# Optimization experiments

Measured on AMD Instinct MI355X. Metric: run time of the kernel, lower is better.

## Reference

```python
import jax, jax.numpy as jnp
import numpy as np

IN_F = 1024
OUT_F = 4096
SEARCH_SPACE = [1, 2, 4, 8, 16]  # block sizes; powers of 2 dividing both dims, capped at 16


def circ_avg(W, bs):
    """Project W [out,in] onto block-circulant structure with block size bs.

    Equivalent to trans_to_cir_meng: within each (bs x bs) block, average each
    wrap-around diagonal and rebuild a circulant block C[k, j] = c[(k - j) % bs].
    """
    q, p = W.shape[0] // bs, W.shape[1] // bs
    t = W.reshape(q, bs, p, bs).transpose(0, 2, 1, 3)  # [q, p, bs, bs]
    i = jnp.arange(bs)
    # rot[..., i, j] = t[..., i, (i + j) % bs]  (rotate rows so diagonals align in columns)
    rot = t[:, :, i[:, None], (i[:, None] + i[None, :]) % bs]  # [q, p, bs, bs]
    c = rot.mean(axis=2)  # [q, p, bs]  mean over each diagonal
    # circulant block: w[..., k, j] = c[..., (k - j) % bs]
    w = c[:, :, (i[:, None] - i[None, :]) % bs]  # [q, p, bs, bs]
    return w.transpose(0, 2, 1, 3).reshape(W.shape)


def setup_inputs() -> dict:
    key = jax.random.key(0)
    k1, k2, k3, k4 = jax.random.split(key, 4)
    x = jax.random.normal(k1, (16, 512, IN_F), dtype=jnp.float32)
    weight = jax.random.normal(k2, (OUT_F, IN_F), dtype=jnp.float32) * 0.02
    alphas = jax.random.normal(k3, (len(SEARCH_SPACE),), dtype=jnp.float32)
    bias = jax.random.normal(k4, (OUT_F,), dtype=jnp.float32) * 0.02
    return {"x": x, "weight": weight, "alphas": alphas, "bias": bias}


def reference(x, weight, alphas, bias):
    # soft NAS mixture over block sizes (tau=1, soft mode)
    a = jax.nn.softmax(alphas)
    W = a[0] * weight  # block_size 1 == original weight
    for idx, bs in enumerate(SEARCH_SPACE[1:], start=1):
        W = W + a[idx] * circ_avg(weight, bs)
    # F.linear: y = x @ W^T + b
    return jnp.einsum("bsi,oi->bso", x, W) + bias
```

## Files before the change

kernel.cpp:

```cpp
#include <hip/hip_runtime.h>

typedef __bf16 bf16;
typedef __bf16 bf16x8 __attribute__((ext_vector_type(8)));
typedef float floatx4 __attribute__((ext_vector_type(4)));

#define IN_F  1024
#define OUT_F 4096
#define M_DIM 8192
#define K_DIM 1024
#define N_DIM 4096

__device__ __forceinline__ unsigned short f2bf(float f) {
    unsigned int u = __float_as_uint(f);
    u += 0x7FFFu + ((u >> 16) & 1u);
    return (unsigned short)(u >> 16);
}

__global__ __launch_bounds__(256) void prep_kernel(
    const float* __restrict__ W, const float* __restrict__ alphas,
    const float* __restrict__ x,
    unsigned short* __restrict__ Wb, uint4* __restrict__ xb)
{
    const int t = threadIdx.x;

    if (blockIdx.x >= 1024) {
        const int g = (blockIdx.x - 1024) * 256 + t;
        const float4* xv = (const float4*)x;
        const float4 v0 = xv[2 * g];
        const float4 v1 = xv[2 * g + 1];
        uint4 o;
        o.x = (unsigned)f2bf(v0.x) | ((unsigned)f2bf(v0.y) << 16);
        o.y = (unsigned)f2bf(v0.z) | ((unsigned)f2bf(v0.w) << 16);
        o.z = (unsigned)f2bf(v1.x) | ((unsigned)f2bf(v1.y) << 16);
        o.w = (unsigned)f2bf(v1.z) | ((unsigned)f2bf(v1.w) << 16);
        xb[g] = o;
        return;
    }

    __shared__ __align__(16) float Wl[16 * 256];
    __shared__ __align__(16) float D2[2048];
    __shared__ float D4[1024];
    __shared__ float D8[512];
    __shared__ float D16[256];

    const int rb = blockIdx.x >> 2;
    const int cb = blockIdx.x & 3;
    const int row0 = rb * 16, col0 = cb * 256;

    const float4* src = (const float4*)(W + (size_t)row0 * IN_F + col0);
    #pragma unroll
    for (int j = 0; j < 4; ++j) {
        const int idx = j * 256 + t;
        const int r = idx >> 6, c4 = idx & 63;
        ((float4*)Wl)[r * 64 + c4] = src[(size_t)r * 256 + c4];
    }

    float av[5];
    float mx = -1e30f;
    #pragma unroll
    for (int j = 0; j < 5; ++j) { av[j] = alphas[j]; mx = fmaxf(mx, av[j]); }
    float s = 0.f;
    #pragma unroll
    for (int j = 0; j < 5; ++j) { av[j] = __expf(av[j] - mx); s += av[j]; }
    const float inv = 1.f / s;
    #pragma unroll
    for (int j = 0; j < 5; ++j) av[j] *= inv;
    #pragma unroll
    for (int e = 1; e <= 4; ++e) av[e] *= 1.0f / (float)(1 << e);

    __syncthreads();

    {   const int c16 = t >> 4, d = t & 15;
        float acc = 0.f;
        #pragma unroll
        for (int r = 0; r < 16; ++r)
            acc += Wl[r * 256 + c16 * 16 + ((r + d) & 15)];
        D16[t] = acc;
    }
    #pragma unroll
    for (int it = 0; it < 2; ++it) {
        const int s8 = t + it * 256;
        const int d = s8 & 7, c8 = (s8 >> 3) & 31, r8 = s8 >> 8;
        float acc = 0.f;
        #pragma unroll
        for (int r = 0; r < 8; ++r)
            acc += Wl[(r8 * 8 + r) * 256 + c8 * 8 + ((r + d) & 7)];
        D8[s8] = acc;
    }
    #pragma unroll
    for (int it = 0; it < 4; ++it) {
        const int s4 = t + it * 256;
        const int d = s4 & 3, c4 = (s4 >> 2) & 63, r4 = s4 >> 8;
        float acc = 0.f;
        #pragma unroll
        for (int r = 0; r < 4; ++r)
            acc += Wl[(r4 * 4 + r) * 256 + c4 * 4 + ((r + d) & 3)];
        D4[s4] = acc;
    }
    #pragma unroll
    for (int it = 0; it < 8; ++it) {
        const int s2 = t + it * 256;
        const int d = s2 & 1, c2 = (s2 >> 1) & 127, r2 = s2 >> 8;
        D2[s2] = Wl[(r2 * 2) * 256 + c2 * 2 + d]
               + Wl[(r2 * 2 + 1) * 256 + c2 * 2 + ((1 + d) & 1)];
    }

    __syncthreads();

    const int k = t >> 4, jj = t & 15;
    float res[16];
    #pragma unroll
    for (int jb = 0; jb < 16; ++jb) {
        const int col = jb * 16 + jj;
        const int dd = k - col;
        res[jb] = av[0] * Wl[k * 256 + col]
                + av[1] * D2[((k >> 1) * 128 + (col >> 1)) * 2 + (dd & 1)]
                + av[2] * D4[((k >> 2) * 64  + (col >> 2)) * 4 + (dd & 3)]
                + av[3] * D8[((k >> 3) * 32  + (col >> 3)) * 8 + (dd & 7)]
                + av[4] * D16[(col >> 4) * 16 + (dd & 15)];
    }

    __syncthreads();
    unsigned short* st = (unsigned short*)D2;
    #pragma unroll
    for (int jb = 0; jb < 16; ++jb)
        st[k * 256 + jb * 16 + jj] = f2bf(res[jb]);
    __syncthreads();

    const uint4* p = (const uint4*)(st + k * 256 + jj * 16);
    uint4* dst = (uint4*)(Wb + (size_t)(row0 + k) * IN_F + col0 + jj * 16);
    dst[0] = p[0];
    dst[1] = p[1];
}

#define GTM 256
#define GTN 128
#define GTK 32
#define A_EL (GTM * GTK)
#define B_EL (GTN * GTK)
#define BUF_EL (A_EL + B_EL)

__global__ __launch_bounds__(256, 2) void gemm_bt_kernel(
    const bf16* __restrict__ A, const bf16* __restrict__ B,
    const float* __restrict__ bias, float* __restrict__ C)
{
    constexpr int N = N_DIM, K = K_DIM;
    constexpr int NT = K / GTK;

    __shared__ __align__(16) bf16 smem[2 * BUF_EL];

    const int t    = threadIdx.x;
    const int w    = t >> 6;
    const int l    = t & 63;
    const int quad = l >> 4;
    const int l16  = l & 15;

    const int wm = (w >> 1) * 128;
    const int wn = (w & 1) * 64;

    const int nb = N / GTN;
    const int bm = blockIdx.x / nb;
    const int bn = blockIdx.x % nb;

    const int fko = l16 * GTK + ((quad ^ ((l16 >> 1) & 3)) * 8);

    const bf16* Ag[4]; int la[4];
    const bf16* Bg[2]; int lb[2];
    {
        const bf16* Abase = A + (size_t)bm * GTM * K;
        const bf16* Bbase = B + (size_t)bn * GTN * K;
        #pragma unroll
        for (int q = 0; q < 4; ++q) {
            const int c = q * 256 + t;
            const int row = c >> 2;
            const int kq = (c & 3) ^ ((row >> 1) & 3);
            Ag[q] = Abase + (size_t)row * K + kq * 8;
            la[q] = (q * 256 + (t & ~63)) * 8;
        }
        #pragma unroll
        for (int q = 0; q < 2; ++q) {
            const int c = q * 256 + t;
            const int row = c >> 2;
            const int kq = (c & 3) ^ ((row >> 1) & 3);
            Bg[q] = Bbase + (size_t)row * K + kq * 8;
            lb[q] = (q * 256 + (t & ~63)) * 8;
        }
    }

    floatx4 acc[8][4] = {};

#define GLL(SRC, DST)                                                         \
    __builtin_amdgcn_global_load_lds(                                         \
        (const __attribute__((address_space(1))) void*)(SRC),                 \
        (__attribute__((address_space(3))) void*)(DST), 16, 0, 0)

#define STAGE(KOFF, BUFP) do {                                                \
        _Pragma("unroll")                                                     \
        for (int q = 0; q < 4; ++q) GLL(Ag[q] + (KOFF), (BUFP) + la[q]);      \
        _Pragma("unroll")                                                     \
        for (int q = 0; q < 2; ++q) GLL(Bg[q] + (KOFF), (BUFP) + A_EL + lb[q]); \
    } while (0)

#define MF(d, va, vb)                                                         \
    d = __builtin_amdgcn_mfma_f32_16x16x32_bf16(va, vb, d, 0, 0, 0)

    STAGE(0, smem);

    #pragma unroll 1
    for (int kt = 0; kt < NT; ++kt) {
        bf16* cur = smem + (kt & 1) * BUF_EL;
        bf16* nxt = smem + ((kt & 1) ^ 1) * BUF_EL;

        if (kt < NT - 1) {
            STAGE((kt + 1) * GTK, nxt);
            asm volatile("s_waitcnt vmcnt(6)" ::: "memory");
        } else {
            asm volatile("s_waitcnt vmcnt(0)" ::: "memory");
        }
        __builtin_amdgcn_s_barrier();

        bf16x8 af[8], bfr[4];
        const bf16* a0 = cur + wm * GTK + fko;
        const bf16* b0 = cur + A_EL + wn * GTK + fko;
        #pragma unroll
        for (int n = 0; n < 4; ++n)
            bfr[n] = *(const bf16x8*)(b0 + n * 16 * GTK);
        #pragma unroll
        for (int m = 0; m < 8; ++m)
            af[m] = *(const bf16x8*)(a0 + m * 16 * GTK);

        __builtin_amdgcn_s_setprio(1);
        #pragma unroll
        for (int m = 0; m < 8; ++m)
            #pragma unroll
            for (int n = 0; n < 4; ++n)
                MF(acc[m][n], af[m], bfr[n]);
        __builtin_amdgcn_s_setprio(0);

        __builtin_amdgcn_s_barrier();
    }
#undef STAGE
#undef GLL
#undef MF

    float bv[4];
    #pragma unroll
    for (int nt = 0; nt < 4; ++nt)
        bv[nt] = bias[bn * GTN + wn + nt * 16 + l16];

    float* Cbase = C + (size_t)(bm * GTM + wm) * N + bn * GTN + wn;
    #pragma unroll
    for (int m = 0; m < 8; ++m) {
        #pragma unroll
        for (int r = 0; r < 4; ++r) {
            float* crowp = Cbase + (size_t)(m * 16 + quad * 4 + r) * N;
            #pragma unroll
            for (int nt = 0; nt < 4; ++nt)
                crowp[nt * 16 + l16] = acc[m][nt][r] + bv[nt];
        }
    }
}

extern "C" void kernel_launch(void* const* d_in, const int* in_sizes, int n_in,
                              void* d_out, int out_size, void* d_ws, size_t ws_size,
                              hipStream_t stream) {
    const float* x      = (const float*)d_in[0];
    const float* weight = (const float*)d_in[1];
    const float* alphas = (const float*)d_in[2];
    const float* bias   = (const float*)d_in[3];
    float* out = (float*)d_out;

    unsigned short* Wb = (unsigned short*)d_ws;
    unsigned short* Xb = (unsigned short*)((char*)d_ws + (size_t)OUT_F * IN_F * 2);

    prep_kernel<<<1024 + 4096, 256, 0, stream>>>(weight, alphas, x, Wb, (uint4*)Xb);

    const int grid = (M_DIM / GTM) * (N_DIM / GTN);
    gemm_bt_kernel<<<grid, 256, 0, stream>>>((const bf16*)Xb, (const bf16*)Wb, bias, out);
}
```

Before: 226.9 us.

## Restructure GEMM into 256x256x64 tiles with 8 waves and staged interleaved prefetch

The bf16 GEMM moves from 256x128x32 tiles with 4 waves to 256x256x64 tiles with 8 waves. The K loop is unrolled into sub-phases that interleave LDS fragment reads, MFMA groups and global-to-LDS prefetch of the next A half-tiles and the B tiles two steps ahead, over a double-buffered 128KB LDS. The goal is more reuse per tile, fewer K iterations and better overlap of loads with matrix math. The cost is many more barriers per tile, and the large LDS footprint combined with launch bounds of 2 may limit occupancy.

```diff
diff --git a/kernel.cpp b/kernel.cpp
--- a/kernel.cpp
+++ b/kernel.cpp
@@ -133,21 +133,17 @@
     dst[1] = p[1];
 }
 
-#define GTM 256
-#define GTN 128
-#define GTK 32
-#define A_EL (GTM * GTK)
-#define B_EL (GTN * GTK)
-#define BUF_EL (A_EL + B_EL)
-
-__global__ __launch_bounds__(256, 2) void gemm_bt_kernel(
+#define BK2 64
+#define HEL 8192
+#define SEL (4 * HEL)
+
+__global__ __launch_bounds__(512, 2) void gemm_bt_kernel(
     const bf16* __restrict__ A, const bf16* __restrict__ B,
     const float* __restrict__ bias, float* __restrict__ C)
 {
     constexpr int N = N_DIM, K = K_DIM;
-    constexpr int NT = K / GTK;
-
-    __shared__ __align__(16) bf16 smem[2 * BUF_EL];
+
+    __shared__ __align__(16) bf16 smem[2 * SEL];
 
     const int t    = threadIdx.x;
     const int w    = t >> 6;
@@ -155,100 +151,119 @@
     const int quad = l >> 4;
     const int l16  = l & 15;
 
-    const int wm = (w >> 1) * 128;
-    const int wn = (w & 1) * 64;
-
-    const int nb = N / GTN;
-    const int bm = blockIdx.x / nb;
-    const int bn = blockIdx.x % nb;
-
-    const int fko = l16 * GTK + ((quad ^ ((l16 >> 1) & 3)) * 8);
-
-    const bf16* Ag[4]; int la[4];
-    const bf16* Bg[2]; int lb[2];
-    {
-        const bf16* Abase = A + (size_t)bm * GTM * K;
-        const bf16* Bbase = B + (size_t)bn * GTN * K;
-        #pragma unroll
-        for (int q = 0; q < 4; ++q) {
-            const int c = q * 256 + t;
-            const int row = c >> 2;
-            const int kq = (c & 3) ^ ((row >> 1) & 3);
-            Ag[q] = Abase + (size_t)row * K + kq * 8;
-            la[q] = (q * 256 + (t & ~63)) * 8;
-        }
-        #pragma unroll
-        for (int q = 0; q < 2; ++q) {
-            const int c = q * 256 + t;
-            const int row = c >> 2;
-            const int kq = (c & 3) ^ ((row >> 1) & 3);
-            Bg[q] = Bbase + (size_t)row * K + kq * 8;
-            lb[q] = (q * 256 + (t & ~63)) * 8;
-        }
-    }
+    const int wr = w >> 2;
+    const int wc = w & 3;
+    const int wm = wr * 128;
+    const int wn = wc * 64;
+
+    const int bm = blockIdx.x >> 4;
+    const int bn = blockIdx.x & 15;
+
+    const int fk0 = ((0 * 4 + quad) ^ (l16 & 7)) * 8;
+    const int fk1 = ((1 * 4 + quad) ^ (l16 & 7)) * 8;
+    const int arow = wr * HEL + l16 * 64;
+    const int brow = (2 + (wc >> 1)) * HEL + ((wc & 1) * 64 + l16) * 64;
+
+    const int r0  = t >> 3;
+    const int kc0 = ((t & 7) ^ (r0 & 7)) * 8;
+    const bf16* pA = A + (size_t)(bm * 256 + r0) * K + kc0;
+    const bf16* pB = B + (size_t)(bn * 256 + r0) * K + kc0;
+    const int t8 = t * 8;
 
     floatx4 acc[8][4] = {};
-
-#define GLL(SRC, DST)                                                         \
+    bf16x8 af[4][2], bfr[4][2];
+
+#define GLL(SRC, DSTOFF)                                                      \
     __builtin_amdgcn_global_load_lds(                                         \
         (const __attribute__((address_space(1))) void*)(SRC),                 \
-        (__attribute__((address_space(3))) void*)(DST), 16, 0, 0)
-
-#define STAGE(KOFF, BUFP) do {                                                \
+        (__attribute__((address_space(3))) void*)(smem + (DSTOFF)), 16, 0, 0)
+
+#define STAGE_A(H, TT, SL) do {                                               \
+    GLL(pA + (size_t)(H) * 128 * K + (TT) * BK2,          (SL) + (H) * HEL + t8);        \
+    GLL(pA + (size_t)(H) * 128 * K + 64 * K + (TT) * BK2, (SL) + (H) * HEL + 4096 + t8); \
+} while (0)
+#define STAGE_B(H, TT, SL) do {                                               \
+    GLL(pB + (size_t)(H) * 128 * K + (TT) * BK2,          (SL) + (2 + (H)) * HEL + t8);        \
+    GLL(pB + (size_t)(H) * 128 * K + 64 * K + (TT) * BK2, (SL) + (2 + (H)) * HEL + 4096 + t8); \
+} while (0)
+
+#define RD_A(MB, SC) do { _Pragma("unroll")                                   \
+    for (int mi = 0; mi < 4; ++mi) {                                          \
+        af[mi][0] = *(const bf16x8*)(smem + (SC) + arow + ((MB) + mi) * 1024 + fk0); \
+        af[mi][1] = *(const bf16x8*)(smem + (SC) + arow + ((MB) + mi) * 1024 + fk1); \
+    } } while (0)
+#define RD_B(NB, SC) do { _Pragma("unroll")                                   \
+    for (int ni = 0; ni < 2; ++ni) {                                          \
+        bfr[(NB) + ni][0] = *(const bf16x8*)(smem + (SC) + brow + ((NB) + ni) * 1024 + fk0); \
+        bfr[(NB) + ni][1] = *(const bf16x8*)(smem + (SC) + brow + ((NB) + ni) * 1024 + fk1); \
+    } } while (0)
+
+#define MFMA16(MB, NB) do {                                                   \
+    __builtin_amdgcn_s_setprio(1);                                            \
+    _Pragma("unroll")                                                         \
+    for (int mi = 0; mi < 4; ++mi)                                            \
         _Pragma("unroll")                                                     \
-        for (int q = 0; q < 4; ++q) GLL(Ag[q] + (KOFF), (BUFP) + la[q]);      \
-        _Pragma("unroll")                                                     \
-        for (int q = 0; q < 2; ++q) GLL(Bg[q] + (KOFF), (BUFP) + A_EL + lb[q]); \
-    } while (0)
-
-#define MF(d, va, vb)                                                         \
-    d = __builtin_amdgcn_mfma_f32_16x16x32_bf16(va, vb, d, 0, 0, 0)
-
-    STAGE(0, smem);
+        for (int ni = 0; ni < 2; ++ni) {                                      \
+            acc[(MB)+mi][(NB)+ni] = __builtin_amdgcn_mfma_f32_16x16x32_bf16(  \
+                af[mi][0], bfr[(NB)+ni][0], acc[(MB)+mi][(NB)+ni], 0, 0, 0);  \
+            acc[(MB)+mi][(NB)+ni] = __builtin_amdgcn_mfma_f32_16x16x32_bf16(  \
+                af[mi][1], bfr[(NB)+ni][1], acc[(MB)+mi][(NB)+ni], 0, 0, 0);  \
+        }                                                                     \
+    __builtin_amdgcn_s_setprio(0);                                            \
+} while (0)
+
+#define BAR() __builtin_amdgcn_s_barrier()
+#define LGKM0() do { asm volatile("s_waitcnt lgkmcnt(0)" ::: "memory");       \
+                     __builtin_amdgcn_sched_barrier(0); } while (0)
+
+#define TILE(TT, SC, SO, DOA, DOB, TRAIL) do {                                \
+                \
+    RD_A(0, SC); RD_B(0, SC); if (DOA) STAGE_A(0, (TT) + 1, SO);              \
+    BAR(); LGKM0(); MFMA16(0, 0); BAR();                                      \
+                                \
+    RD_B(2, SC); if (DOA) STAGE_A(1, (TT) + 1, SO);                           \
+    BAR(); LGKM0(); MFMA16(0, 2); BAR();                                      \
+      \
+    RD_A(4, SC); if (DOB) STAGE_B(0, (TT) + 2, SC);                           \
+    BAR(); LGKM0(); MFMA16(4, 0); BAR();                                      \
+                                     \
+    if (DOB) STAGE_B(1, (TT) + 2, SC);                                        \
+    BAR(); MFMA16(4, 2);                                                      \
+    TRAIL; BAR();                                                             \
+} while (0)
+
+    STAGE_B(0, 0, 0);   STAGE_B(1, 0, 0);
+    STAGE_A(0, 0, 0);   STAGE_A(1, 0, 0);
+    STAGE_B(0, 1, SEL); STAGE_B(1, 1, SEL);
+    asm volatile("s_waitcnt vmcnt(4)" ::: "memory");
+    BAR();
 
     #pragma unroll 1
-    for (int kt = 0; kt < NT; ++kt) {
-        bf16* cur = smem + (kt & 1) * BUF_EL;
-        bf16* nxt = smem + ((kt & 1) ^ 1) * BUF_EL;
-
-        if (kt < NT - 1) {
-            STAGE((kt + 1) * GTK, nxt);
-            asm volatile("s_waitcnt vmcnt(6)" ::: "memory");
-        } else {
-            asm volatile("s_waitcnt vmcnt(0)" ::: "memory");
-        }
-        __builtin_amdgcn_s_barrier();
-
-        bf16x8 af[8], bfr[4];
-        const bf16* a0 = cur + wm * GTK + fko;
-        const bf16* b0 = cur + A_EL + wn * GTK + fko;
-        #pragma unroll
-        for (int n = 0; n < 4; ++n)
-            bfr[n] = *(const bf16x8*)(b0 + n * 16 * GTK);
-        #pragma unroll
-        for (int m = 0; m < 8; ++m)
-            af[m] = *(const bf16x8*)(a0 + m * 16 * GTK);
-
-        __builtin_amdgcn_s_setprio(1);
-        #pragma unroll
-        for (int m = 0; m < 8; ++m)
-            #pragma unroll
-            for (int n = 0; n < 4; ++n)
-                MF(acc[m][n], af[m], bfr[n]);
-        __builtin_amdgcn_s_setprio(0);
-
-        __builtin_amdgcn_s_barrier();
-    }
-#undef STAGE
+    for (int T = 0; T < 12; T += 2) {
+        TILE(T,     0,   SEL, true, true, asm volatile("s_waitcnt vmcnt(4)" ::: "memory"));
+        TILE(T + 1, SEL, 0,   true, true, asm volatile("s_waitcnt vmcnt(4)" ::: "memory"));
+    }
+    TILE(12, 0,   SEL, true,  true,  asm volatile("s_waitcnt vmcnt(4)" ::: "memory"));
+    TILE(13, SEL, 0,   true,  true,  asm volatile("s_waitcnt vmcnt(4)" ::: "memory"));
+    TILE(14, 0,   SEL, true,  false, asm volatile("s_waitcnt vmcnt(0)" ::: "memory"));
+    TILE(15, SEL, 0,   false, false, (void)0);
+
+#undef TILE
+#undef LGKM0
+#undef BAR
+#undef MFMA16
+#undef RD_B
+#undef RD_A
+#undef STAGE_B
+#undef STAGE_A
 #undef GLL
-#undef MF
 
     float bv[4];
     #pragma unroll
     for (int nt = 0; nt < 4; ++nt)
-        bv[nt] = bias[bn * GTN + wn + nt * 16 + l16];
-
-    float* Cbase = C + (size_t)(bm * GTM + wm) * N + bn * GTN + wn;
+        bv[nt] = bias[bn * 256 + wn + nt * 16 + l16];
+
+    float* Cbase = C + (size_t)(bm * 256 + wm) * N + bn * 256 + wn;
     #pragma unroll
     for (int m = 0; m < 8; ++m) {
         #pragma unroll
@@ -275,6 +290,6 @@
 
     prep_kernel<<<1024 + 4096, 256, 0, stream>>>(weight, alphas, x, Wb, (uint4*)Xb);
 
-    const int grid = (M_DIM / GTM) * (N_DIM / GTN);
-    gemm_bt_kernel<<<grid, 256, 0, stream>>>((const bf16*)Xb, (const bf16*)Wb, bias, out);
-}
+    const int grid = (M_DIM / 256) * (N_DIM / 256);
+    gemm_bt_kernel<<<grid, 512, 0, stream>>>((const bf16*)Xb, (const bf16*)Wb, bias, out);
+}
```

Result: no change. 224.0 us (-1.3%).
